# Performance work log

Measured on AMD Instinct MI355X. Metric: run time of the kernel, lower is better.

## Reference

```python
import jax, jax.numpy as jnp
import numpy as np

NH = 12      # bert-base heads
NL = 32      # num_latents
K = 64       # hard-coded topk in forward


def _ln(x, g, b):
    m = x.mean(-1, keepdims=True)
    v = ((x - m) ** 2).mean(-1, keepdims=True)
    return (x - m) / jnp.sqrt(v + 1e-12) * g + b


def _attn(xq, xkv, w, b, mask_add=None):
    # w: [4,H,H] (q,k,v,o), b: [4,H]
    B, Lq, H = xq.shape
    dh = H // NH
    q = (xq @ w[0] + b[0]).reshape(B, Lq, NH, dh)
    k = (xkv @ w[1] + b[1]).reshape(B, -1, NH, dh)
    v = (xkv @ w[2] + b[2]).reshape(B, -1, NH, dh)
    s = jnp.einsum('bqhd,bkhd->bhqk', q, k) / np.sqrt(dh).astype(xq.dtype)
    if mask_add is not None:
        s = s + mask_add
    p = jax.nn.softmax(s, axis=-1)          # [B,NH,Lq,Lk]
    o = jnp.einsum('bhqk,bkhd->bqhd', p, v).reshape(B, Lq, H)
    return o @ w[3] + b[3], p


def _cross_block(q, enc, w, b, g, lb, mask_add=None):
    # w:[L,8,H,H]; per layer: self-attn+LN then cross-attn+LN (FFN stripped)
    p_last = None
    for l in range(w.shape[0]):
        a, _ = _attn(q, q, w[l, :4], b[l, :4])
        q = _ln(q + a, g[l, 0], lb[l, 0])
        a, p_last = _attn(q, enc, w[l, 4:], b[l, 4:], mask_add)
        q = _ln(q + a, g[l, 1], lb[l, 1])
    return q, p_last


def _self_block(q, w, b, g, lb):
    probs = []
    for l in range(w.shape[0]):
        a, p = _attn(q, q, w[l], b[l])
        q = _ln(q + a, g[l, 0], lb[l, 0])
        probs.append(p)
    return q, jnp.concatenate(probs, axis=1)  # concat over head dim like torch.concat(attentions, dim=1)


def setup_inputs() -> dict:
    key = jax.random.key(0)
    ks = jax.random.split(key, 24)
    B, S, T, H, L = 32, 1024, 64, 768, 2
    std = 0.02
    inp = {
        'audio_embeds': jax.random.normal(ks[0], (B, S, H), jnp.float32),
        'text_embeds': jax.random.normal(ks[1], (B, T, H), jnp.float32),
        'attention_mask': jnp.ones((B, T), jnp.int32),
        'audio_qt': jax.random.normal(ks[2], (1, NL, H), jnp.float32) * std,
        'text_qt': jax.random.normal(ks[3], (1, NL, H), jnp.float32) * std,
    }
    for i, pre in enumerate(['tm', 'am', 'mg']):
        inp[pre + '_w'] = jax.random.normal(ks[4 + i], (L, 8, H, H), jnp.float32) * std
        inp[pre + '_b'] = jnp.zeros((L, 8, H), jnp.float32)
        inp[pre + '_g'] = jnp.ones((L, 2, H), jnp.float32)
        inp[pre + '_lb'] = jnp.zeros((L, 2, H), jnp.float32)
    inp['sel_w'] = jax.random.normal(ks[8], (L, 4, H, H), jnp.float32) * std
    inp['sel_b'] = jnp.zeros((L, 4, H), jnp.float32)
    inp['sel_g'] = jnp.ones((L, 1, H), jnp.float32)
    inp['sel_lb'] = jnp.zeros((L, 1, H), jnp.float32)
    return inp


def reference(audio_embeds, text_embeds, audio_qt, text_qt,
              tm_w, tm_b, tm_g, tm_lb, am_w, am_b, am_g, am_lb,
              sel_w, sel_b, sel_g, sel_lb, mg_w, mg_b, mg_g, mg_lb,
              attention_mask):
    B, S, H = audio_embeds.shape
    mask_add = (1.0 - attention_mask.astype(audio_embeds.dtype))[:, None, None, :] * -1e4

    # text token merger
    latent_text, _ = _cross_block(jnp.broadcast_to(text_qt, (B, NL, H)), text_embeds,
                                  tm_w, tm_b, tm_g, tm_lb, mask_add)
    # audio token merger (capture last-layer cross-attn probs)
    latent_audio, cross_p = _cross_block(jnp.broadcast_to(audio_qt, (B, NL, H)), audio_embeds,
                                         am_w, am_b, am_g, am_lb)
    latent_attention_score = cross_p.mean(axis=1)          # [B,NL,S]

    latent = jnp.concatenate([latent_audio, latent_text], axis=1)  # [B,2NL,H]
    fused, attn_all = _self_block(latent, sel_w, sel_b, sel_g, sel_lb)  # attn_all [B,L*NH,2NL,2NL]
    aas = attn_all[:, :, :NL, NL:].mean(axis=1)            # [B,NL,NL]

    imp = jnp.einsum('bqk,bks->bqs', aas, latent_attention_score).mean(axis=1)  # [B,S]
    _, idx = jax.lax.top_k(imp, K)
    sorted_idx = jnp.sort(idx, axis=1)                     # [B,K]

    sel_mask = jnp.zeros((B, S), bool).at[jnp.arange(B)[:, None], sorted_idx].set(True)
    q_tokens = jnp.take_along_axis(audio_embeds, sorted_idx[..., None], axis=1)  # [B,K,H]
    unsel_idx = jnp.argsort(sel_mask, axis=1, stable=True)[:, :S - K]            # order-preserving
    kv_rest = jnp.take_along_axis(audio_embeds, unsel_idx[..., None], axis=1)    # [B,S-K,H]
    kv = jnp.concatenate([kv_rest, fused], axis=1)                               # [B,S,H]

    out, _ = _cross_block(q_tokens, kv, mg_w, mg_b, mg_g, mg_lb)
    return out
```

## Files before the change

kernel.cpp:

```cpp
#include <hip/hip_runtime.h>
#include <hip/hip_bf16.h>
#include <math.h>

namespace {
constexpr int kB = 32, kS = 1024, kT = 64, kH = 768, kNH = 12, kDH = 64;
constexpr int kNL = 32, kTopK = 64, kL = 2;
constexpr size_t kMat = (size_t)kH * kH;
}

typedef _Float16 half8 __attribute__((ext_vector_type(8)));
typedef float floatx4 __attribute__((ext_vector_type(4)));

#define AS1U(p) ((const __attribute__((address_space(1))) unsigned int*)(p))
#define AS3U(p) ((__attribute__((address_space(3))) unsigned int*)(p))

__device__ __forceinline__ void split_write(float v, _Float16* H, _Float16* L, size_t i) {
    _Float16 h = (_Float16)v;
    H[i] = h;
    L[i] = (_Float16)(v - (float)h);
}

template<int NP>
__global__ __launch_bounds__(256) void gemm16(
    const _Float16* __restrict__ Aqh, const _Float16* __restrict__ Aql,
// ... 107 lines not shown
    const _Float16* __restrict__ Ah_, const _Float16* __restrict__ Al_,
    const _Float16* __restrict__ Bh_, const _Float16* __restrict__ Bl_,
    const float* __restrict__ bias, float* __restrict__ Y, int M)
{
    constexpr int NPL = (NP == 3) ? 4 : 2;
    __shared__ _Float16 lds[NPL * 4096];
    const int tid = threadIdx.x;
    const int lane = tid & 63, wave = tid >> 6;
    const size_t rm = (size_t)blockIdx.x * 128;
    const size_t cn = (size_t)blockIdx.y * 128;
    const int wr = (wave >> 1) * 64, wc = (wave & 1) * 64;

    const int lrow = lane >> 2;
    const int lchunk = (lane & 3) ^ ((lane >> 3) & 3);
    const int q = lane >> 4;
    const int fr = lane & 15;
    const int rslot = q ^ ((fr >> 1) & 3);

    const _Float16* gsrc;
    _Float16* lbase;
    int jbase;
    if constexpr (NP == 3) {
        gsrc = (wave == 0) ? Ah_ + rm * kH : (wave == 1) ? Al_ + rm * kH
             : (wave == 2) ? Bh_ + cn * kH : Bl_ + cn * kH;
        lbase = &lds[wave * 4096];
        jbase = 0;
    } else {
        gsrc = (wave < 2) ? Ah_ + rm * kH : Bh_ + cn * kH;
        lbase = &lds[(wave >> 1) * 4096];
        jbase = (wave & 1) * 4;
    }
    constexpr int CPW = (NP == 3) ? 8 : 4;

    floatx4 acc[4][4] = {};
    for (int k0 = 0; k0 < kH; k0 += 32) {
        #pragma unroll
        for (int c = 0; c < CPW; ++c) {
            int j = jbase + c;
            const _Float16* src = gsrc + (size_t)(j * 16 + lrow) * kH + k0 + lchunk * 8;
            _Float16* dst = lbase + j * 512 + lane * 8;
            __builtin_amdgcn_global_load_lds(AS1U(src), AS3U(dst), 16, 0, 0);
        }
        __syncthreads();
        half8 ah[4], bh[4], al[4], bl[4];
        #pragma unroll
        for (int m = 0; m < 4; ++m) {
            int r = wr + m * 16 + fr;
            ah[m] = *(const half8*)&lds[r * 32 + rslot * 8];
            if constexpr (NP == 3) al[m] = *(const half8*)&lds[4096 + r * 32 + rslot * 8];
        }
        constexpr int pb = (NP == 3) ? 2 : 1;
        #pragma unroll
        for (int n = 0; n < 4; ++n) {
            int r = wc + n * 16 + fr;
            bh[n] = *(const half8*)&lds[pb * 4096 + r * 32 + rslot * 8];
            if constexpr (NP == 3) bl[n] = *(const half8*)&lds[3 * 4096 + r * 32 + rslot * 8];
        }
        #pragma unroll
        for (int m = 0; m < 4; ++m)
            #pragma unroll
            for (int n = 0; n < 4; ++n) {
                acc[m][n] = __builtin_amdgcn_mfma_f32_16x16x32_f16(ah[m], bh[n], acc[m][n], 0, 0, 0);
                if constexpr (NP == 3) {
                    acc[m][n] = __builtin_amdgcn_mfma_f32_16x16x32_f16(ah[m], bl[n], acc[m][n], 0, 0, 0);
                    acc[m][n] = __builtin_amdgcn_mfma_f32_16x16x32_f16(al[m], bh[n], acc[m][n], 0, 0, 0);
                }
            }
        __syncthreads();
    }
    #pragma unroll
    for (int m = 0; m < 4; ++m) {
        int row0 = wr + m * 16 + (lane >> 4) * 4;
        #pragma unroll
        for (int n = 0; n < 4; ++n) {
            int col = (int)cn + wc + n * 16 + fr;
            float bv = bias[col];
            #pragma unroll
            for (int j = 0; j < 4; ++j)
                Y[(rm + row0 + j) * (size_t)kH + col] = acc[m][n][j] + bv;
        }
    }
}

template<int NP>
__global__ __launch_bounds__(256) void attn_big(
    const _Float16* __restrict__ Qh, const _Float16* __restrict__ Ql,
    const _Float16* __restrict__ Kh, const _Float16* __restrict__ Kl,
    float* __restrict__ P, int Lq, int Lk)
{
    constexpr int NPL = (NP == 3) ? 2 : 1;
    const int tid = threadIdx.x, lane = tid & 63, wave = tid >> 6;
    const int fr = lane & 15, part = lane >> 4;
    const int bh = blockIdx.x, b = bh / kNH, h = bh % kNH;
    const int q0 = blockIdx.y * 32;
    const int key0 = wave * 256;
    __shared__ float red[32][4];

    half8 qa[2][2][NPL];
    #pragma unroll
    for (int m = 0; m < 2; ++m)
        #pragma unroll
        for (int c = 0; c < 2; ++c) {
            size_t ro = (size_t)(b * Lq + q0 + m * 16 + fr) * kH + h * kDH + c * 32 + part * 8;
            qa[m][c][0] = *(const half8*)&Qh[ro];
            if constexpr (NP == 3) qa[m][c][1] = *(const half8*)&Ql[ro];
        }
    floatx4 acc[2][16] = {};
    #pragma unroll
    for (int n = 0; n < 16; ++n)
        #pragma unroll
        for (int c = 0; c < 2; ++c) {
            size_t ro = (size_t)(b * Lk + key0 + n * 16 + fr) * kH + h * kDH + c * 32 + part * 8;
            half8 kh8 = *(const half8*)&Kh[ro];
            half8 kl8;
            if constexpr (NP == 3) kl8 = *(const half8*)&Kl[ro];
            #pragma unroll
            for (int m = 0; m < 2; ++m) {
                acc[m][n] = __builtin_amdgcn_mfma_f32_16x16x32_f16(qa[m][c][0], kh8, acc[m][n], 0, 0, 0);
                if constexpr (NP == 3) {
                    acc[m][n] = __builtin_amdgcn_mfma_f32_16x16x32_f16(qa[m][c][0], kl8, acc[m][n], 0, 0, 0);
                    acc[m][n] = __builtin_amdgcn_mfma_f32_16x16x32_f16(qa[m][c][1], kh8, acc[m][n], 0, 0, 0);
                }
            }
        }
    #pragma unroll
    for (int m = 0; m < 2; ++m)
        #pragma unroll
        for (int n = 0; n < 16; ++n)
            #pragma unroll
            for (int j = 0; j < 4; ++j) acc[m][n][j] *= 0.125f;
    #pragma unroll
    for (int m = 0; m < 2; ++m)
        #pragma unroll
        for (int j = 0; j < 4; ++j) {
            float v = acc[m][0][j];
            #pragma unroll
            for (int n = 1; n < 16; ++n) v = fmaxf(v, acc[m][n][j]);
            #pragma unroll
            for (int o = 1; o < 16; o <<= 1) v = fmaxf(v, __shfl_xor(v, o));
            red[m * 16 + part * 4 + j][wave] = v;
        }
    __syncthreads();
    float gm[2][4];
    #pragma unroll
    for (int m = 0; m < 2; ++m)
        #pragma unroll
        for (int j = 0; j < 4; ++j) {
            int r = m * 16 + part * 4 + j;
            gm[m][j] = fmaxf(fmaxf(red[r][0], red[r][1]), fmaxf(red[r][2], red[r][3]));
        }
    __syncthreads();
    #pragma unroll
    for (int m = 0; m < 2; ++m)
        #pragma unroll
        for (int j = 0; j < 4; ++j) {
            float s = 0.f;
            #pragma unroll
            for (int n = 0; n < 16; ++n) {
                float e = expf(acc[m][n][j] - gm[m][j]);
                acc[m][n][j] = e;
                s += e;
            }
            #pragma unroll
            for (int o = 1; o < 16; o <<= 1) s += __shfl_xor(s, o);
            red[m * 16 + part * 4 + j][wave] = s;
        }
    __syncthreads();
    #pragma unroll
    for (int m = 0; m < 2; ++m)
        #pragma unroll
        for (int j = 0; j < 4; ++j) {
            int r = m * 16 + part * 4 + j;
            float inv = 1.0f / (red[r][0] + red[r][1] + red[r][2] + red[r][3]);
            size_t rowbase = ((size_t)bh * Lq + q0 + m * 16 + part * 4 + j) * Lk + key0;
            #pragma unroll
            for (int n = 0; n < 16; ++n)
                P[rowbase + n * 16 + fr] = acc[m][n][j] * inv;
        }
}

template<int LQ, int NP>
__global__ __launch_bounds__((LQ / 16) * 64) void pv_mfma(
    const float* __restrict__ P,
    const _Float16* __restrict__ Vh, const _Float16* __restrict__ Vl,
    _Float16* __restrict__ Oh, _Float16* __restrict__ Ol, int Lk)
{
    constexpr int NW = LQ / 16, NT = NW * 64;
    constexpr int NPL = (NP == 3) ? 2 : 1;
    __shared__ _Float16 vT[NPL][64][72];
    const int tid = threadIdx.x, lane = tid & 63, wave = tid >> 6;
    const int fr = lane & 15, part = lane >> 4;
    const int bh = blockIdx.x, b = bh / kNH, h = bh % kNH;
    const int qbase = wave * 16;

    floatx4 acc[4] = {};
    for (int kb = 0; kb < Lk; kb += 64) {
        for (int idx = tid; idx < 64 * 8; idx += NT) {
            int r = idx >> 3, c8 = idx & 7;
            half8 v = *(const half8*)&Vh[(size_t)(b * Lk + kb + r) * kH + h * kDH + c8 * 8];
            #pragma unroll
            for (int e = 0; e < 8; ++e) vT[0][c8 * 8 + e][r] = v[e];
            if constexpr (NP == 3) {
                half8 w = *(const half8*)&Vl[(size_t)(b * Lk + kb + r) * kH + h * kDH + c8 * 8];
                #pragma unroll
                for (int e = 0; e < 8; ++e) vT[1][c8 * 8 + e][r] = w[e];
            }
        }
        __syncthreads();
        half8 pa[2][NPL];
        #pragma unroll
        for (int c = 0; c < 2; ++c) {
            const float* src = &P[((size_t)bh * LQ + qbase + fr) * Lk + kb + c * 32 + part * 8];
            float4 x = *(const float4*)src, y = *(const float4*)(src + 4);
            float vv[8] = {x.x, x.y, x.z, x.w, y.x, y.y, y.z, y.w};
            #pragma unroll
            for (int e = 0; e < 8; ++e) {
                _Float16 hh = (_Float16)vv[e];
                pa[c][0][e] = hh;
                if constexpr (NP == 3) pa[c][1][e] = (_Float16)(vv[e] - (float)hh);
            }
        }
        #pragma unroll
        for (int n = 0; n < 4; ++n)
            #pragma unroll
            for (int c = 0; c < 2; ++c) {
                half8 bh8 = *(const half8*)&vT[0][n * 16 + fr][c * 32 + part * 8];
                acc[n] = __builtin_amdgcn_mfma_f32_16x16x32_f16(pa[c][0], bh8, acc[n], 0, 0, 0);
                if constexpr (NP == 3) {
                    half8 bl8 = *(const half8*)&vT[1][n * 16 + fr][c * 32 + part * 8];
                    acc[n] = __builtin_amdgcn_mfma_f32_16x16x32_f16(pa[c][0], bl8, acc[n], 0, 0, 0);
                    acc[n] = __builtin_amdgcn_mfma_f32_16x16x32_f16(pa[c][1], bh8, acc[n], 0, 0, 0);
                }
            }
        __syncthreads();
    }
    #pragma unroll
    for (int n = 0; n < 4; ++n)
        #pragma unroll
        for (int j = 0; j < 4; ++j) {
            size_t oi = (size_t)(b * LQ + qbase + part * 4 + j) * kH + h * kDH + n * 16 + fr;
            float v = acc[n][j];
            _Float16 hh = (_Float16)v;
            Oh[oi] = hh;
            if constexpr (NP == 3) Ol[oi] = (_Float16)(v - (float)hh);
        }
}

template<int LQ, int LK, int NP, bool MASKED, bool CAPTURE>
__global__ __launch_bounds__((LQ / 16) * 64) void attn_small(
    const _Float16* Qh, const _Float16* Ql,
    const _Float16* __restrict__ Kh, const _Float16* __restrict__ Kl,
    const _Float16* __restrict__ Vh, const _Float16* __restrict__ Vl,
    _Float16* Oh, _Float16* Ol,
    float* __restrict__ Pcap, const int* __restrict__ amask)
{
    constexpr int NW = LQ / 16, NT = NW * 64, NN = LK / 16, NC = LK / 32;
    constexpr int NPL = (NP == 3) ? 2 : 1;
    constexpr int PIT = LK + 8;
    __shared__ _Float16 vT[NPL][64][PIT];
    __shared__ _Float16 Pld[NW][NPL][16][PIT];
    const int tid = threadIdx.x, lane = tid & 63, wave = tid >> 6;
    const int fr = lane & 15, part = lane >> 4;
    const int bh = blockIdx.x, b = bh / kNH, h = bh % kNH;

    for (int idx = tid; idx < LK * 8; idx += NT) {
        int r = idx >> 3, c8 = idx & 7;
        half8 v = *(const half8*)&Vh[(size_t)(b * LK + r) * kH + h * kDH + c8 * 8];
        #pragma unroll
        for (int e = 0; e < 8; ++e) vT[0][c8 * 8 + e][r] = v[e];
        if constexpr (NP == 3) {
            half8 w = *(const half8*)&Vl[(size_t)(b * LK + r) * kH + h * kDH + c8 * 8];
            #pragma unroll
            for (int e = 0; e < 8; ++e) vT[1][c8 * 8 + e][r] = w[e];
        }
    }
    half8 qa[2][NPL];
    #pragma unroll
    for (int c = 0; c < 2; ++c) {
        size_t ro = (size_t)(b * LQ + wave * 16 + fr) * kH + h * kDH + c * 32 + part * 8;
        qa[c][0] = *(const half8*)&Qh[ro];
        if constexpr (NP == 3) qa[c][1] = *(const half8*)&Ql[ro];
    }
    floatx4 acc[NN] = {};
    #pragma unroll
    for (int n = 0; n < NN; ++n)
        #pragma unroll
        for (int c = 0; c < 2; ++c) {
            size_t ro = (size_t)(b * LK + n * 16 + fr) * kH + h * kDH + c * 32 + part * 8;
            half8 kh8 = *(const half8*)&Kh[ro];
            acc[n] = __builtin_amdgcn_mfma_f32_16x16x32_f16(qa[c][0], kh8, acc[n], 0, 0, 0);
            if constexpr (NP == 3) {
                half8 kl8 = *(const half8*)&Kl[ro];
                acc[n] = __builtin_amdgcn_mfma_f32_16x16x32_f16(qa[c][0], kl8, acc[n], 0, 0, 0);
                acc[n] = __builtin_amdgcn_mfma_f32_16x16x32_f16(qa[c][1], kh8, acc[n], 0, 0, 0);
            }
        }
    #pragma unroll
    for (int n = 0; n < NN; ++n) {
        float madd = 0.f;
        if constexpr (MASKED)
            madd = (1.0f - (float)amask[b * kT + n * 16 + fr]) * -1e4f;
        #pragma unroll
        for (int j = 0; j < 4; ++j) acc[n][j] = acc[n][j] * 0.125f + madd;
    }
    #pragma unroll
    for (int j = 0; j < 4; ++j) {
        float m = acc[0][j];
        #pragma unroll
        for (int n = 1; n < NN; ++n) m = fmaxf(m, acc[n][j]);
        #pragma unroll
        for (int o = 1; o < 16; o <<= 1) m = fmaxf(m, __shfl_xor(m, o));
        float s = 0.f;
        #pragma unroll
        for (int n = 0; n < NN; ++n) { float e = expf(acc[n][j] - m); acc[n][j] = e; s += e; }
        #pragma unroll
        for (int o = 1; o < 16; o <<= 1) s += __shfl_xor(s, o);
        float inv = 1.0f / s;
        #pragma unroll
        for (int n = 0; n < NN; ++n) acc[n][j] *= inv;
    }
    #pragma unroll
    for (int n = 0; n < NN; ++n)
        #pragma unroll
        for (int j = 0; j < 4; ++j) {
// ... 205 lines not shown
    for (int c = threadIdx.x; c < kH; c += 256) {
        float v = qt[(size_t)n * kH + c];
        q[(size_t)bn * kH + c] = v;
        split_write(v, Qh, Ql, (size_t)bn * kH + c);
    }
}

__global__ __launch_bounds__(256) void concat_lat(const float* __restrict__ qa,
    const float* __restrict__ qt, float* __restrict__ lat,
    _Float16* __restrict__ Lh, _Float16* __restrict__ Ll)
{
    const int br = blockIdx.x;
    const int b = br >> 6, r = br & 63;
    const float* src = (r < kNL) ? qa + (size_t)(b * kNL + r) * kH
                                 : qt + (size_t)(b * kNL + (r - kNL)) * kH;
    for (int c = threadIdx.x; c < kH; c += 256) {
        float v = src[c];
        lat[(size_t)br * kH + c] = v;
        split_write(v, Lh, Ll, (size_t)br * kH + c);
    }
}

__global__ __launch_bounds__(256) void gather_q(const float* __restrict__ audio,
    const int* __restrict__ selidx, float* __restrict__ qm,
    _Float16* __restrict__ Qh, _Float16* __restrict__ Ql)
{
    const int bj = blockIdx.x;
    const int b = bj >> 6;
    const int srow = selidx[bj];
    const float* src = audio + ((size_t)b * kS + srow) * kH;
    for (int c = threadIdx.x; c < kH; c += 256) {
        float v = src[c];
        qm[(size_t)bj * kH + c] = v;
        split_write(v, Qh, Ql, (size_t)bj * kH + c);
    }
}

__global__ __launch_bounds__(256) void build_kv(const float* __restrict__ audio,
    const float* __restrict__ fused, const int* __restrict__ unselidx,
    _Float16* __restrict__ Kh, _Float16* __restrict__ Kl)
{
    const int br = blockIdx.x;
    const int b = br >> 10, r = br & 1023;
    const float* src;
    if (r < kS - kTopK) src = audio + ((size_t)b * kS + unselidx[b * (kS - kTopK) + r]) * kH;
    else                src = fused + (size_t)(b * kTopK + (r - (kS - kTopK))) * kH;
    for (int c = threadIdx.x; c < kH; c += 256)
        split_write(src[c], Kh, Kl, (size_t)br * kH + c);
}

extern "C" void kernel_launch(void* const* d_in, const int* in_sizes, int n_in,
                              void* d_out, int out_size, void* d_ws, size_t ws_size,
                              hipStream_t stream)
{
    const float* audio    = (const float*)d_in[0];
    const float* text     = (const float*)d_in[1];
    const int*   amask    = (const int*)  d_in[2];
    const float* audio_qt = (const float*)d_in[3];
    const float* text_qt  = (const float*)d_in[4];
    const float* tm_w  = (const float*)d_in[5];
    const float* tm_b  = (const float*)d_in[6];
    const float* tm_g  = (const float*)d_in[7];
    const float* tm_lb = (const float*)d_in[8];
    const float* am_w  = (const float*)d_in[9];
    const float* am_b  = (const float*)d_in[10];
    const float* am_g  = (const float*)d_in[11];
    const float* am_lb = (const float*)d_in[12];
    const float* mg_w  = (const float*)d_in[13];
    const float* mg_b  = (const float*)d_in[14];
    const float* mg_g  = (const float*)d_in[15];
    const float* mg_lb = (const float*)d_in[16];
    const float* sel_w  = (const float*)d_in[17];
    const float* sel_b  = (const float*)d_in[18];
    const float* sel_g  = (const float*)d_in[19];
    const float* sel_lb = (const float*)d_in[20];
    (void)in_sizes; (void)n_in; (void)out_size;

    char* base = (char*)d_ws;
    size_t off = 0;
    auto alloc = [&](size_t bytes) {
        off = (off + 255) & ~(size_t)255;
        void* p = base + off; off += bytes; return p;
    };
    float* Pbuf   = (float*)alloc((size_t)kB * kNH * 64 * kS * 4);
    float* attA   = (float*)alloc((size_t)2048 * kH * 4);
    float* q_text = (float*)alloc((size_t)1024 * kH * 4);
    float* q_audio= (float*)alloc((size_t)1024 * kH * 4);
    float* latent = (float*)alloc((size_t)2048 * kH * 4);
    float* qmerge = (float*)alloc((size_t)2048 * kH * 4);
    float* latsc  = (float*)alloc((size_t)kB * kNL * kS * 4);
    float* aas    = (float*)alloc((size_t)kB * kNL * kNL * 4);
    float* impb   = (float*)alloc((size_t)kB * kS * 4);
    int* selidx   = (int*)alloc((size_t)kB * kTopK * 4);
    int* unselidx = (int*)alloc((size_t)kB * (kS - kTopK) * 4);
    _Float16* Wh  = (_Float16*)alloc(16 * kMat * 2);
    _Float16* Wl  = (_Float16*)alloc(16 * kMat * 2);
    _Float16* BGh = (_Float16*)alloc((size_t)kB * kS * kH * 2);
    _Float16* BGl = (_Float16*)alloc((size_t)kB * kS * kH * 2);
    _Float16* PTh = (_Float16*)alloc((size_t)kB * kT * kH * 2);
    _Float16* PTl = (_Float16*)alloc((size_t)kB * kT * kH * 2);
    _Float16* PLqh= (_Float16*)alloc((size_t)2048 * kH * 2);
    _Float16* PLql= (_Float16*)alloc((size_t)2048 * kH * 2);
    _Float16* PLoh= (_Float16*)alloc((size_t)2048 * kH * 2);
    _Float16* PLol= (_Float16*)alloc((size_t)2048 * kH * 2);
    _Float16* KVh = (_Float16*)alloc((size_t)kB * kS * kH * 2);
    _Float16* KVl = (_Float16*)alloc((size_t)kB * kS * kH * 2);
    if (off > ws_size) return;

    _Float16* Qh = PLoh;
    _Float16* Ql = PLol;

    auto attn = [&](const float* qf, int Lq,
                    const _Float16* qah, const _Float16* qal,
                    const _Float16* eah, const _Float16* eal, int Lk,
                    int wmat, const float* bias, const float* g, const float* lb,
                    const int* mask, int capture, bool np3,
                    float* q_out, _Float16* oh, _Float16* ol)
    {
        const int Mq = kB * Lq, Mk = kB * Lk;
        const _Float16* WhB = Wh + (size_t)wmat * kMat;
        const _Float16* WlB = Wl + (size_t)wmat * kMat;
        const int gx = (Mq > Mk ? Mq : Mk) / 128;
        if (Lk >= 256) {
            dim3 g1(gx, 6, 2);
            if (np3) gemm16<3><<<g1, 256, 0, stream>>>(qah, qal, eah, eal, WhB, WlB, bias,
                         Qh, Ql, KVh, KVl, nullptr, nullptr, Mq, Mk);
            else     gemm16<1><<<g1, 256, 0, stream>>>(qah, qal, eah, eal, WhB, WlB, bias,
                         Qh, Ql, KVh, KVl, nullptr, nullptr, Mq, Mk);
            dim3 g2(kB * kNH, Lq / 32);
            if (np3) attn_big<3><<<g2, 256, 0, stream>>>(Qh, Ql, KVh, KVl, Pbuf, Lq, Lk);
            else     attn_big<1><<<g2, 256, 0, stream>>>(Qh, Ql, KVh, KVl, Pbuf, Lq, Lk);
            if (capture == 1) mean_heads<<<kB * kNL, 256, 0, stream>>>(Pbuf, latsc);
            dim3 g3(Mk / 128, 6, 1);
            if (np3) gemm16<3><<<g3, 256, 0, stream>>>(eah, eal, eah, eal,
                         WhB + 2 * kMat, WlB + 2 * kMat, bias + 2 * kH,
                         KVh, KVl, nullptr, nullptr, nullptr, nullptr, Mk, Mk);
            else     gemm16<1><<<g3, 256, 0, stream>>>(eah, eal, eah, eal,
                         WhB + 2 * kMat, WlB + 2 * kMat, bias + 2 * kH,
                         KVh, KVl, nullptr, nullptr, nullptr, nullptr, Mk, Mk);
            if (Lq == 32) {
                if (np3) pv_mfma<32, 3><<<kB * kNH, 128, 0, stream>>>(Pbuf, KVh, KVl, PLoh, PLol, Lk);
                else     pv_mfma<32, 1><<<kB * kNH, 128, 0, stream>>>(Pbuf, KVh, KVl, PLoh, PLol, Lk);
            } else {
                if (np3) pv_mfma<64, 3><<<kB * kNH, 256, 0, stream>>>(Pbuf, KVh, KVl, PLoh, PLol, Lk);
                else     pv_mfma<64, 1><<<kB * kNH, 256, 0, stream>>>(Pbuf, KVh, KVl, PLoh, PLol, Lk);
            }
        } else {
            _Float16* V2h = KVh + (size_t)Mk * kH;
            _Float16* V2l = KVl + (size_t)Mk * kH;
            dim3 g1(gx, 6, 3);
            if (np3) gemm16<3><<<g1, 256, 0, stream>>>(qah, qal, eah, eal, WhB, WlB, bias,
                         Qh, Ql, KVh, KVl, V2h, V2l, Mq, Mk);
            else     gemm16<1><<<g1, 256, 0, stream>>>(qah, qal, eah, eal, WhB, WlB, bias,
                         Qh, Ql, KVh, KVl, V2h, V2l, Mq, Mk);
            if (Lq == 32 && Lk == 32)
                attn_small<32, 32, 3, false, false><<<kB * kNH, 128, 0, stream>>>(
                    Qh, Ql, KVh, KVl, V2h, V2l, PLoh, PLol, nullptr, nullptr);
            else if (Lq == 32 && Lk == 64)
                attn_small<32, 64, 3, true, false><<<kB * kNH, 128, 0, stream>>>(
                    Qh, Ql, KVh, KVl, V2h, V2l, PLoh, PLol, nullptr, mask);
            else if (np3)
                attn_small<64, 64, 3, false, true><<<kB * kNH, 256, 0, stream>>>(
                    Qh, Ql, KVh, KVl, V2h, V2l, PLoh, PLol, Pbuf, nullptr);
            else
                attn_small<64, 64, 1, false, false><<<kB * kNH, 256, 0, stream>>>(
                    Qh, Ql, KVh, KVl, V2h, V2l, PLoh, PLol, nullptr, nullptr);
            if (capture == 2)      aas_acc<<<kB, 256, 0, stream>>>(Pbuf, aas, 1);
            else if (capture == 3) aas_acc<<<kB, 256, 0, stream>>>(Pbuf, aas, 0);
        }
        dim3 g4(Mq / 128, 6);
        if (np3) gemm_o32<3><<<g4, 256, 0, stream>>>(PLoh, PLol, WhB + 3 * kMat, WlB + 3 * kMat,
                     bias + 3 * kH, attA, Mq);
        else     gemm_o32<1><<<g4, 256, 0, stream>>>(PLoh, PLol, WhB + 3 * kMat, WlB + 3 * kMat,
                     bias + 3 * kH, attA, Mq);
        ln_residual<<<Mq, 256, 0, stream>>>(qf, attA, g, lb, q_out, oh, ol);
    };

    split2<<<(kB * kT * kH) / 1024, 256, 0, stream>>>(text, PTh, PTl, kB * kT * kH);
    split2<<<(kB * kS * kH) / 1024, 256, 0, stream>>>(audio, BGh, BGl, kB * kS * kH);

    wconv<<<dim3(24, 24, 16), 256, 0, stream>>>(tm_w, Wh, Wl);
    bcast_q<<<kB * kNL, 256, 0, stream>>>(text_qt, q_text, PLqh, PLql);
    for (int l = 0; l < kL; ++l) {
        attn(q_text, kNL, PLqh, PLql, PLqh, PLql, kNL, l * 8 + 0,
             tm_b + (size_t)l * 8 * kH, tm_g + (size_t)l * 2 * kH, tm_lb + (size_t)l * 2 * kH,
             nullptr, 0, true, q_text, PLqh, PLql);
        attn(q_text, kNL, PLqh, PLql, PTh, PTl, kT, l * 8 + 4,
             tm_b + ((size_t)l * 8 + 4) * kH, tm_g + ((size_t)l * 2 + 1) * kH, tm_lb + ((size_t)l * 2 + 1) * kH,
             amask, 0, true, q_text, PLqh, PLql);
    }
    wconv<<<dim3(24, 24, 16), 256, 0, stream>>>(am_w, Wh, Wl);
    bcast_q<<<kB * kNL, 256, 0, stream>>>(audio_qt, q_audio, PLqh, PLql);
    for (int l = 0; l < kL; ++l) {
        attn(q_audio, kNL, PLqh, PLql, PLqh, PLql, kNL, l * 8 + 0,
             am_b + (size_t)l * 8 * kH, am_g + (size_t)l * 2 * kH, am_lb + (size_t)l * 2 * kH,
             nullptr, 0, true, q_audio, PLqh, PLql);
        attn(q_audio, kNL, PLqh, PLql, BGh, BGl, kS, l * 8 + 4,
             am_b + ((size_t)l * 8 + 4) * kH, am_g + ((size_t)l * 2 + 1) * kH, am_lb + ((size_t)l * 2 + 1) * kH,
             nullptr, (l == kL - 1) ? 1 : 0, true, q_audio, PLqh, PLql);
    }
    concat_lat<<<kB * 64, 256, 0, stream>>>(q_audio, q_text, latent, PLqh, PLql);
    wconv<<<dim3(24, 24, 8), 256, 0, stream>>>(sel_w, Wh, Wl);
    for (int l = 0; l < kL; ++l) {
        attn(latent, 64, PLqh, PLql, PLqh, PLql, 64, l * 4,
             sel_b + (size_t)l * 4 * kH, sel_g + (size_t)l * kH, sel_lb + (size_t)l * kH,
             nullptr, (l == 0) ? 2 : 3, true, latent, PLqh, PLql);
    }
    imp_kernel<<<kB, 256, 0, stream>>>(aas, latsc, impb);
    topk_kernel<<<kB, 256, 0, stream>>>(impb, selidx, unselidx);
    gather_q<<<kB * kTopK, 256, 0, stream>>>(audio, selidx, qmerge, PLqh, PLql);
    build_kv<<<kB * kS, 256, 0, stream>>>(audio, latent, unselidx, BGh, BGl);
    wconv<<<dim3(24, 24, 16), 256, 0, stream>>>(mg_w, Wh, Wl);
    for (int l = 0; l < kL; ++l) {
        attn(qmerge, 64, PLqh, PLql, PLqh, PLql, 64, l * 8 + 0,
             mg_b + (size_t)l * 8 * kH, mg_g + (size_t)l * 2 * kH, mg_lb + (size_t)l * 2 * kH,
             nullptr, 0, false, qmerge, PLqh, PLql);
        float* qo = (l == kL - 1) ? (float*)d_out : qmerge;
        _Float16* oh = (l == kL - 1) ? nullptr : PLqh;
        _Float16* ol = (l == kL - 1) ? nullptr : PLql;
        attn(qmerge, 64, PLqh, PLql, BGh, BGl, kS, l * 8 + 4,
             mg_b + ((size_t)l * 8 + 4) * kH, mg_g + ((size_t)l * 2 + 1) * kH, mg_lb + ((size_t)l * 2 + 1) * kH,
             nullptr, 0, false, qo, oh, ol);
    }
}
```

Measured before the change: 2.338 ms.

## Reassociate cross-attention to skip K/V projections of the long sequence

For the two cross-attention stages over the 1024-token sequence, the K and V projections of the encoder sequence are replaced by reassociated products. The per-head query is folded through Wk (R = Q_h·Wk_hᵀ) and scored directly against the raw encoder embeddings. P is multiplied by the raw embeddings first and then by Wv. This removes the large Mk×768×768 K and V GEMMs in exchange for per-head 64×768 intermediates and extra small GEMMs. K-bias is dropped, which is valid because it shifts every score in a row equally, and V-bias is added after the projection, which is valid because softmax rows sum to one. The merge stage also stores P in fp16 to halve its traffic, which may change accuracy.

```diff
diff --git a/kernel.cpp b/kernel.cpp
--- a/kernel.cpp
+++ b/kernel.cpp
@@ -213,47 +213,96 @@
     }
 }
 
-template<int NP>
-__global__ __launch_bounds__(256) void attn_big(
+template<int LQ, int NP>
+__global__ __launch_bounds__(256) void rgemm(
     const _Float16* __restrict__ Qh, const _Float16* __restrict__ Ql,
-    const _Float16* __restrict__ Kh, const _Float16* __restrict__ Kl,
-    float* __restrict__ P, int Lq, int Lk)
-{
-    constexpr int NPL = (NP == 3) ? 2 : 1;
+    const _Float16* __restrict__ Wnh, const _Float16* __restrict__ Wnl,
+    _Float16* __restrict__ Rh, _Float16* __restrict__ Rl)
+{
+    constexpr int MM = LQ / 16;
     const int tid = threadIdx.x, lane = tid & 63, wave = tid >> 6;
     const int fr = lane & 15, part = lane >> 4;
     const int bh = blockIdx.x, b = bh / kNH, h = bh % kNH;
+    const int ncol = blockIdx.y * 64 + wave * 16;
+
+    half8 qa[MM][2][2];
+    #pragma unroll
+    for (int m = 0; m < MM; ++m)
+        #pragma unroll
+        for (int c = 0; c < 2; ++c) {
+            size_t ro = (size_t)(b * LQ + m * 16 + fr) * kH + h * kDH + c * 32 + part * 8;
+            qa[m][c][0] = *(const half8*)&Qh[ro];
+            if constexpr (NP == 3) qa[m][c][1] = *(const half8*)&Ql[ro];
+        }
+    floatx4 acc[MM] = {};
+    #pragma unroll
+    for (int c = 0; c < 2; ++c) {
+        size_t ro = (size_t)(ncol + fr) * kH + h * kDH + c * 32 + part * 8;
+        half8 wb = *(const half8*)&Wnh[ro];
+        half8 wl;
+        if constexpr (NP == 3) wl = *(const half8*)&Wnl[ro];
+        #pragma unroll
+        for (int m = 0; m < MM; ++m) {
+            acc[m] = __builtin_amdgcn_mfma_f32_16x16x32_f16(qa[m][c][0], wb, acc[m], 0, 0, 0);
+            if constexpr (NP == 3) {
+                acc[m] = __builtin_amdgcn_mfma_f32_16x16x32_f16(qa[m][c][0], wl, acc[m], 0, 0, 0);
+                acc[m] = __builtin_amdgcn_mfma_f32_16x16x32_f16(qa[m][c][1], wb, acc[m], 0, 0, 0);
+            }
+        }
+    }
+    #pragma unroll
+    for (int m = 0; m < MM; ++m)
+        #pragma unroll
+        for (int j = 0; j < 4; ++j) {
+            size_t oi = (size_t)(bh * LQ + m * 16 + part * 4 + j) * kH + ncol + fr;
+            float v = acc[m][j];
+            _Float16 hh = (_Float16)v;
+            Rh[oi] = hh;
+            if constexpr (NP == 3) Rl[oi] = (_Float16)(v - (float)hh);
+        }
+}
+
+template<int NP, bool PF16>
+__global__ __launch_bounds__(256) void scores_rx(
+    const _Float16* __restrict__ Rh, const _Float16* __restrict__ Rl,
+    const _Float16* __restrict__ Xh, const _Float16* __restrict__ Xl,
+    float* __restrict__ P32, _Float16* __restrict__ P16, int Lq)
+{
+    const int tid = threadIdx.x, lane = tid & 63, wave = tid >> 6;
+    const int fr = lane & 15, part = lane >> 4;
+    const int i = blockIdx.x;
+    const int b = (i & 7) * 4 + ((i >> 3) & 3);
+    const int h = i >> 5;
+    const int bh = b * kNH + h;
     const int q0 = blockIdx.y * 32;
     const int key0 = wave * 256;
     __shared__ float red[32][4];
 
-    half8 qa[2][2][NPL];
-    #pragma unroll
-    for (int m = 0; m < 2; ++m)
-        #pragma unroll
-        for (int c = 0; c < 2; ++c) {
-            size_t ro = (size_t)(b * Lq + q0 + m * 16 + fr) * kH + h * kDH + c * 32 + part * 8;
-            qa[m][c][0] = *(const half8*)&Qh[ro];
-            if constexpr (NP == 3) qa[m][c][1] = *(const half8*)&Ql[ro];
-        }
     floatx4 acc[2][16] = {};
-    #pragma unroll
-    for (int n = 0; n < 16; ++n)
-        #pragma unroll
-        for (int c = 0; c < 2; ++c) {
-            size_t ro = (size_t)(b * Lk + key0 + n * 16 + fr) * kH + h * kDH + c * 32 + part * 8;
-            half8 kh8 = *(const half8*)&Kh[ro];
-            half8 kl8;
-            if constexpr (NP == 3) kl8 = *(const half8*)&Kl[ro];
+    for (int c = 0; c < 24; ++c) {
+        half8 ah[2][2];
+        #pragma unroll
+        for (int m = 0; m < 2; ++m) {
+            size_t ro = (size_t)(bh * Lq + q0 + m * 16 + fr) * kH + c * 32 + part * 8;
+            ah[m][0] = *(const half8*)&Rh[ro];
+            if constexpr (NP == 3) ah[m][1] = *(const half8*)&Rl[ro];
+        }
+        #pragma unroll
+        for (int n = 0; n < 16; ++n) {
+            size_t ro = (size_t)(b * kS + key0 + n * 16 + fr) * kH + c * 32 + part * 8;
+            half8 bh8 = *(const half8*)&Xh[ro];
+            half8 bl8;
+            if constexpr (NP == 3) bl8 = *(const half8*)&Xl[ro];
             #pragma unroll
             for (int m = 0; m < 2; ++m) {
-                acc[m][n] = __builtin_amdgcn_mfma_f32_16x16x32_f16(qa[m][c][0], kh8, acc[m][n], 0, 0, 0);
+                acc[m][n] = __builtin_amdgcn_mfma_f32_16x16x32_f16(ah[m][0], bh8, acc[m][n], 0, 0, 0);
                 if constexpr (NP == 3) {
-                    acc[m][n] = __builtin_amdgcn_mfma_f32_16x16x32_f16(qa[m][c][0], kl8, acc[m][n], 0, 0, 0);
-                    acc[m][n] = __builtin_amdgcn_mfma_f32_16x16x32_f16(qa[m][c][1], kh8, acc[m][n], 0, 0, 0);
+                    acc[m][n] = __builtin_amdgcn_mfma_f32_16x16x32_f16(ah[m][0], bl8, acc[m][n], 0, 0, 0);
+                    acc[m][n] = __builtin_amdgcn_mfma_f32_16x16x32_f16(ah[m][1], bh8, acc[m][n], 0, 0, 0);
                 }
             }
         }
+    }
     #pragma unroll
     for (int m = 0; m < 2; ++m)
         #pragma unroll
@@ -303,74 +352,138 @@
         for (int j = 0; j < 4; ++j) {
             int r = m * 16 + part * 4 + j;
             float inv = 1.0f / (red[r][0] + red[r][1] + red[r][2] + red[r][3]);
-            size_t rowbase = ((size_t)bh * Lq + q0 + m * 16 + part * 4 + j) * Lk + key0;
-            #pragma unroll
-            for (int n = 0; n < 16; ++n)
-                P[rowbase + n * 16 + fr] = acc[m][n][j] * inv;
-        }
+            size_t rowbase = ((size_t)bh * Lq + q0 + m * 16 + part * 4 + j) * kS + key0;
+            #pragma unroll
+            for (int n = 0; n < 16; ++n) {
+                float p = acc[m][n][j] * inv;
+                if constexpr (PF16) P16[rowbase + n * 16 + fr] = (_Float16)p;
+                else                P32[rowbase + n * 16 + fr] = p;
+            }
+        }
+}
+
+template<int LQ, int NP, bool PF16>
+__global__ __launch_bounds__(256) void zgemm(
+    const float* __restrict__ P32, const _Float16* __restrict__ P16,
+    const _Float16* __restrict__ Xh, const _Float16* __restrict__ Xl,
+    _Float16* __restrict__ Zh, _Float16* __restrict__ Zl)
+{
+    constexpr int MM = LQ / 16;
+    constexpr int NPL = (NP == 3) ? 2 : 1;
+    __shared__ _Float16 xT[NPL][128][72];
+    const int tid = threadIdx.x, lane = tid & 63, wave = tid >> 6;
+    const int fr = lane & 15, part = lane >> 4;
+    const int i = blockIdx.x;
+    const int b = (i & 7) * 4 + ((i >> 3) & 3);
+    const int r2 = i >> 5;
+    const int h = r2 % kNH, nt = r2 / kNH;
+    const int bh = b * kNH + h;
+
+    floatx4 acc[MM][2] = {};
+    for (int kb = 0; kb < 16; ++kb) {
+        for (int idx = tid; idx < 64 * 16; idx += 256) {
+            int key = idx >> 4, cg = idx & 15;
+            size_t ro = (size_t)(b * kS + kb * 64 + key) * kH + nt * 128 + cg * 8;
+            half8 v = *(const half8*)&Xh[ro];
+            #pragma unroll
+            for (int e = 0; e < 8; ++e) xT[0][cg * 8 + e][key] = v[e];
+            if constexpr (NP == 3) {
+                half8 w = *(const half8*)&Xl[ro];
+                #pragma unroll
+                for (int e = 0; e < 8; ++e) xT[1][cg * 8 + e][key] = w[e];
+            }
+        }
+        __syncthreads();
+        #pragma unroll
+        for (int c2 = 0; c2 < 2; ++c2) {
+            half8 pa[MM][2];
+            #pragma unroll
+            for (int m = 0; m < MM; ++m) {
+                if constexpr (PF16) {
+                    size_t ro = (size_t)(bh * LQ + m * 16 + fr) * kS + kb * 64 + c2 * 32 + part * 8;
+                    pa[m][0] = *(const half8*)&P16[ro];
+                } else {
+                    const float* src = &P32[(size_t)(bh * LQ + m * 16 + fr) * kS + kb * 64 + c2 * 32 + part * 8];
+                    float4 x = *(const float4*)src, y = *(const float4*)(src + 4);
+                    float vv[8] = {x.x, x.y, x.z, x.w, y.x, y.y, y.z, y.w};
+                    #pragma unroll
+                    for (int e = 0; e < 8; ++e) {
+                        _Float16 hh = (_Float16)vv[e];
+                        pa[m][0][e] = hh;
+                        if constexpr (NP == 3) pa[m][1][e] = (_Float16)(vv[e] - (float)hh);
+                    }
+                }
+            }
+            #pragma unroll
+            for (int nf = 0; nf < 2; ++nf) {
+                int col = wave * 32 + nf * 16 + fr;
+                half8 bh8 = *(const half8*)&xT[0][col][c2 * 32 + part * 8];
+                half8 bl8;
+                if constexpr (NP == 3) bl8 = *(const half8*)&xT[1][col][c2 * 32 + part * 8];
+                #pragma unroll
+                for (int m = 0; m < MM; ++m) {
+                    acc[m][nf] = __builtin_amdgcn_mfma_f32_16x16x32_f16(pa[m][0], bh8, acc[m][nf], 0, 0, 0);
+                    if constexpr (NP == 3) {
+                        acc[m][nf] = __builtin_amdgcn_mfma_f32_16x16x32_f16(pa[m][0], bl8, acc[m][nf], 0, 0, 0);
+                        acc[m][nf] = __builtin_amdgcn_mfma_f32_16x16x32_f16(pa[m][1], bh8, acc[m][nf], 0, 0, 0);
+                    }
+                }
+            }
+        }
+        __syncthreads();
+    }
+    #pragma unroll
+    for (int m = 0; m < MM; ++m)
+        #pragma unroll
+        for (int nf = 0; nf < 2; ++nf)
+            #pragma unroll
+            for (int j = 0; j < 4; ++j) {
+                size_t oi = (size_t)(bh * LQ + m * 16 + part * 4 + j) * kH + nt * 128 + wave * 32 + nf * 16 + fr;
+                float v = acc[m][nf][j];
+                _Float16 hh = (_Float16)v;
+                Zh[oi] = hh;
+                if constexpr (NP == 3) Zl[oi] = (_Float16)(v - (float)hh);
+            }
 }
 
 template<int LQ, int NP>
-__global__ __launch_bounds__((LQ / 16) * 64) void pv_mfma(
-    const float* __restrict__ P,
-    const _Float16* __restrict__ Vh, const _Float16* __restrict__ Vl,
-    _Float16* __restrict__ Oh, _Float16* __restrict__ Ol, int Lk)
-{
-    constexpr int NW = LQ / 16, NT = NW * 64;
-    constexpr int NPL = (NP == 3) ? 2 : 1;
-    __shared__ _Float16 vT[NPL][64][72];
+__global__ __launch_bounds__(256) void ogemm(
+    const _Float16* __restrict__ Zh, const _Float16* __restrict__ Zl,
+    const _Float16* __restrict__ WTh, const _Float16* __restrict__ WTl,
+    const float* __restrict__ bv,
+    _Float16* __restrict__ Oh, _Float16* __restrict__ Ol)
+{
+    constexpr int MM = LQ / 16;
     const int tid = threadIdx.x, lane = tid & 63, wave = tid >> 6;
     const int fr = lane & 15, part = lane >> 4;
     const int bh = blockIdx.x, b = bh / kNH, h = bh % kNH;
-    const int qbase = wave * 16;
-
-    floatx4 acc[4] = {};
-    for (int kb = 0; kb < Lk; kb += 64) {
-        for (int idx = tid; idx < 64 * 8; idx += NT) {
-            int r = idx >> 3, c8 = idx & 7;
-            half8 v = *(const half8*)&Vh[(size_t)(b * Lk + kb + r) * kH + h * kDH + c8 * 8];
-            #pragma unroll
-            for (int e = 0; e < 8; ++e) vT[0][c8 * 8 + e][r] = v[e];
+    const int colbase = h * kDH + wave * 16;
+
+    floatx4 acc[MM] = {};
+    for (int c = 0; c < 24; ++c) {
+        size_t wo = (size_t)(colbase + fr) * kH + c * 32 + part * 8;
+        half8 wb = *(const half8*)&WTh[wo];
+        half8 wl;
+        if constexpr (NP == 3) wl = *(const half8*)&WTl[wo];
+        #pragma unroll
+        for (int m = 0; m < MM; ++m) {
+            size_t ro = (size_t)(bh * LQ + m * 16 + fr) * kH + c * 32 + part * 8;
+            half8 ah = *(const half8*)&Zh[ro];
+            acc[m] = __builtin_amdgcn_mfma_f32_16x16x32_f16(ah, wb, acc[m], 0, 0, 0);
             if constexpr (NP == 3) {
-                half8 w = *(const half8*)&Vl[(size_t)(b * Lk + kb + r) * kH + h * kDH + c8 * 8];
-                #pragma unroll
-                for (int e = 0; e < 8; ++e) vT[1][c8 * 8 + e][r] = w[e];
-            }
-        }
-        __syncthreads();
-        half8 pa[2][NPL];
-        #pragma unroll
-        for (int c = 0; c < 2; ++c) {
-            const float* src = &P[((size_t)bh * LQ + qbase + fr) * Lk + kb + c * 32 + part * 8];
-            float4 x = *(const float4*)src, y = *(const float4*)(src + 4);
-            float vv[8] = {x.x, x.y, x.z, x.w, y.x, y.y, y.z, y.w};
-            #pragma unroll
-            for (int e = 0; e < 8; ++e) {
-                _Float16 hh = (_Float16)vv[e];
-                pa[c][0][e] = hh;
-                if constexpr (NP == 3) pa[c][1][e] = (_Float16)(vv[e] - (float)hh);
-            }
-        }
-        #pragma unroll
-        for (int n = 0; n < 4; ++n)
-            #pragma unroll
-            for (int c = 0; c < 2; ++c) {
-                half8 bh8 = *(const half8*)&vT[0][n * 16 + fr][c * 32 + part * 8];
-                acc[n] = __builtin_amdgcn_mfma_f32_16x16x32_f16(pa[c][0], bh8, acc[n], 0, 0, 0);
-                if constexpr (NP == 3) {
-                    half8 bl8 = *(const half8*)&vT[1][n * 16 + fr][c * 32 + part * 8];
-                    acc[n] = __builtin_amdgcn_mfma_f32_16x16x32_f16(pa[c][0], bl8, acc[n], 0, 0, 0);
-                    acc[n] = __builtin_amdgcn_mfma_f32_16x16x32_f16(pa[c][1], bh8, acc[n], 0, 0, 0);
-                }
-            }
-        __syncthreads();
-    }
-    #pragma unroll
-    for (int n = 0; n < 4; ++n)
+                half8 al = *(const half8*)&Zl[ro];
+                acc[m] = __builtin_amdgcn_mfma_f32_16x16x32_f16(ah, wl, acc[m], 0, 0, 0);
+                acc[m] = __builtin_amdgcn_mfma_f32_16x16x32_f16(al, wb, acc[m], 0, 0, 0);
+            }
+        }
+    }
+    float bias = bv[colbase + fr];
+    #pragma unroll
+    for (int m = 0; m < MM; ++m)
         #pragma unroll
         for (int j = 0; j < 4; ++j) {
-            size_t oi = (size_t)(b * LQ + qbase + part * 4 + j) * kH + h * kDH + n * 16 + fr;
-            float v = acc[n][j];
+            size_t oi = (size_t)(b * LQ + m * 16 + part * 4 + j) * kH + colbase + fr;
+            float v = acc[m][j] + bias;
             _Float16 hh = (_Float16)v;
             Oh[oi] = hh;
             if constexpr (NP == 3) Ol[oi] = (_Float16)(v - (float)hh);
@@ -742,7 +855,7 @@
         off = (off + 255) & ~(size_t)255;
         void* p = base + off; off += bytes; return p;
     };
-    float* Pbuf   = (float*)alloc((size_t)kB * kNH * 64 * kS * 4);
+    float* Pbuf   = (float*)alloc((size_t)kB * kNH * 32 * kS * 4);
     float* attA   = (float*)alloc((size_t)2048 * kH * 4);
     float* q_text = (float*)alloc((size_t)1024 * kH * 4);
     float* q_audio= (float*)alloc((size_t)1024 * kH * 4);
@@ -755,6 +868,8 @@
     int* unselidx = (int*)alloc((size_t)kB * (kS - kTopK) * 4);
     _Float16* Wh  = (_Float16*)alloc(16 * kMat * 2);
     _Float16* Wl  = (_Float16*)alloc(16 * kMat * 2);
+    _Float16* WkNh= (_Float16*)alloc(2 * kMat * 2);
+    _Float16* WkNl= (_Float16*)alloc(2 * kMat * 2);
     _Float16* BGh = (_Float16*)alloc((size_t)kB * kS * kH * 2);
     _Float16* BGl = (_Float16*)alloc((size_t)kB * kS * kH * 2);
     _Float16* PTh = (_Float16*)alloc((size_t)kB * kT * kH * 2);
@@ -763,8 +878,10 @@
     _Float16* PLql= (_Float16*)alloc((size_t)2048 * kH * 2);
     _Float16* PLoh= (_Float16*)alloc((size_t)2048 * kH * 2);
     _Float16* PLol= (_Float16*)alloc((size_t)2048 * kH * 2);
-    _Float16* KVh = (_Float16*)alloc((size_t)kB * kS * kH * 2);
-    _Float16* KVl = (_Float16*)alloc((size_t)kB * kS * kH * 2);
+    _Float16* KVh = (_Float16*)alloc((size_t)2 * 2048 * kH * 2);
+    _Float16* KVl = (_Float16*)alloc((size_t)2 * 2048 * kH * 2);
+    _Float16* ZRh = (_Float16*)alloc((size_t)kB * kNH * 64 * kH * 2);
+    _Float16* ZRl = (_Float16*)alloc((size_t)kB * kNH * 64 * kH * 2);
     if (off > ws_size) return;
 
     _Float16* Qh = PLoh;
@@ -781,53 +898,70 @@
         const _Float16* WhB = Wh + (size_t)wmat * kMat;
         const _Float16* WlB = Wl + (size_t)wmat * kMat;
         const int gx = (Mq > Mk ? Mq : Mk) / 128;
-        if (Lk >= 256) {
-            dim3 g1(gx, 6, 2);
-            if (np3) gemm16<3><<<g1, 256, 0, stream>>>(qah, qal, eah, eal, WhB, WlB, bias,
-                         Qh, Ql, KVh, KVl, nullptr, nullptr, Mq, Mk);
-            else     gemm16<1><<<g1, 256, 0, stream>>>(qah, qal, eah, eal, WhB, WlB, bias,
-                         Qh, Ql, KVh, KVl, nullptr, nullptr, Mq, Mk);
-            dim3 g2(kB * kNH, Lq / 32);
-            if (np3) attn_big<3><<<g2, 256, 0, stream>>>(Qh, Ql, KVh, KVl, Pbuf, Lq, Lk);
-            else     attn_big<1><<<g2, 256, 0, stream>>>(Qh, Ql, KVh, KVl, Pbuf, Lq, Lk);
-            if (capture == 1) mean_heads<<<kB * kNL, 256, 0, stream>>>(Pbuf, latsc);
-            dim3 g3(Mk / 128, 6, 1);
-            if (np3) gemm16<3><<<g3, 256, 0, stream>>>(eah, eal, eah, eal,
-                         WhB + 2 * kMat, WlB + 2 * kMat, bias + 2 * kH,
-                         KVh, KVl, nullptr, nullptr, nullptr, nullptr, Mk, Mk);
-            else     gemm16<1><<<g3, 256, 0, stream>>>(eah, eal, eah, eal,
-                         WhB + 2 * kMat, WlB + 2 * kMat, bias + 2 * kH,
-                         KVh, KVl, nullptr, nullptr, nullptr, nullptr, Mk, Mk);
-            if (Lq == 32) {
-                if (np3) pv_mfma<32, 3><<<kB * kNH, 128, 0, stream>>>(Pbuf, KVh, KVl, PLoh, PLol, Lk);
-                else     pv_mfma<32, 1><<<kB * kNH, 128, 0, stream>>>(Pbuf, KVh, KVl, PLoh, PLol, Lk);
-            } else {
-                if (np3) pv_mfma<64, 3><<<kB * kNH, 256, 0, stream>>>(Pbuf, KVh, KVl, PLoh, PLol, Lk);
-                else     pv_mfma<64, 1><<<kB * kNH, 256, 0, stream>>>(Pbuf, KVh, KVl, PLoh, PLol, Lk);
-            }
-        } else {
-            _Float16* V2h = KVh + (size_t)Mk * kH;
-            _Float16* V2l = KVl + (size_t)Mk * kH;
-            dim3 g1(gx, 6, 3);
-            if (np3) gemm16<3><<<g1, 256, 0, stream>>>(qah, qal, eah, eal, WhB, WlB, bias,
-                         Qh, Ql, KVh, KVl, V2h, V2l, Mq, Mk);
-            else     gemm16<1><<<g1, 256, 0, stream>>>(qah, qal, eah, eal, WhB, WlB, bias,
-                         Qh, Ql, KVh, KVl, V2h, V2l, Mq, Mk);
-            if (Lq == 32 && Lk == 32)
-                attn_small<32, 32, 3, false, false><<<kB * kNH, 128, 0, stream>>>(
-                    Qh, Ql, KVh, KVl, V2h, V2l, PLoh, PLol, nullptr, nullptr);
-            else if (Lq == 32 && Lk == 64)
-                attn_small<32, 64, 3, true, false><<<kB * kNH, 128, 0, stream>>>(
-                    Qh, Ql, KVh, KVl, V2h, V2l, PLoh, PLol, nullptr, mask);
-            else if (np3)
-                attn_small<64, 64, 3, false, true><<<kB * kNH, 256, 0, stream>>>(
-                    Qh, Ql, KVh, KVl, V2h, V2l, PLoh, PLol, Pbuf, nullptr);
-            else
-                attn_small<64, 64, 1, false, false><<<kB * kNH, 256, 0, stream>>>(
-                    Qh, Ql, KVh, KVl, V2h, V2l, PLoh, PLol, nullptr, nullptr);
-            if (capture == 2)      aas_acc<<<kB, 256, 0, stream>>>(Pbuf, aas, 1);
-            else if (capture == 3) aas_acc<<<kB, 256, 0, stream>>>(Pbuf, aas, 0);
-        }
+        _Float16* V2h = KVh + (size_t)Mk * kH;
+        _Float16* V2l = KVl + (size_t)Mk * kH;
+        dim3 g1(gx, 6, 3);
+        if (np3) gemm16<3><<<g1, 256, 0, stream>>>(qah, qal, eah, eal, WhB, WlB, bias,
+                     Qh, Ql, KVh, KVl, V2h, V2l, Mq, Mk);
+        else     gemm16<1><<<g1, 256, 0, stream>>>(qah, qal, eah, eal, WhB, WlB, bias,
+                     Qh, Ql, KVh, KVl, V2h, V2l, Mq, Mk);
+        if (Lq == 32 && Lk == 32)
+            attn_small<32, 32, 3, false, false><<<kB * kNH, 128, 0, stream>>>(
+                Qh, Ql, KVh, KVl, V2h, V2l, PLoh, PLol, nullptr, nullptr);
+        else if (Lq == 32 && Lk == 64)
+            attn_small<32, 64, 3, true, false><<<kB * kNH, 128, 0, stream>>>(
+                Qh, Ql, KVh, KVl, V2h, V2l, PLoh, PLol, nullptr, mask);
+        else if (np3)
+            attn_small<64, 64, 3, false, true><<<kB * kNH, 256, 0, stream>>>(
+                Qh, Ql, KVh, KVl, V2h, V2l, PLoh, PLol, Pbuf, nullptr);
+        else
+            attn_small<64, 64, 1, false, false><<<kB * kNH, 256, 0, stream>>>(
+                Qh, Ql, KVh, KVl, V2h, V2l, PLoh, PLol, nullptr, nullptr);
+        if (capture == 2)      aas_acc<<<kB, 256, 0, stream>>>(Pbuf, aas, 1);
+        else if (capture == 3) aas_acc<<<kB, 256, 0, stream>>>(Pbuf, aas, 0);
+        dim3 g4(Mq / 128, 6);
+        if (np3) gemm_o32<3><<<g4, 256, 0, stream>>>(PLoh, PLol, WhB + 3 * kMat, WlB + 3 * kMat,
+                     bias + 3 * kH, attA, Mq);
+        else     gemm_o32<1><<<g4, 256, 0, stream>>>(PLoh, PLol, WhB + 3 * kMat, WlB + 3 * kMat,
+                     bias + 3 * kH, attA, Mq);
+        ln_residual<<<Mq, 256, 0, stream>>>(qf, attA, g, lb, q_out, oh, ol);
+    };
+
+    auto big_step = [&](const float* qf, int Lq,
+                        const _Float16* qah, const _Float16* qal,
+                        int wmat, int kl, const float* bias,
+                        const float* g, const float* lb,
+                        int capture, bool np3,
+                        float* q_out, _Float16* oh, _Float16* ol)
+    {
+        const int Mq = kB * Lq;
+        const _Float16* WhB = Wh + (size_t)wmat * kMat;
+        const _Float16* WlB = Wl + (size_t)wmat * kMat;
+        dim3 gq(Mq / 128, 6, 1);
+        if (np3) gemm16<3><<<gq, 256, 0, stream>>>(qah, qal, qah, qal, WhB, WlB, bias,
+                     Qh, Ql, nullptr, nullptr, nullptr, nullptr, Mq, Mq);
+        else     gemm16<1><<<gq, 256, 0, stream>>>(qah, qal, qah, qal, WhB, WlB, bias,
+                     Qh, Ql, nullptr, nullptr, nullptr, nullptr, Mq, Mq);
+        dim3 gr(kB * kNH, 12);
+        if (np3) rgemm<32, 3><<<gr, 256, 0, stream>>>(Qh, Ql, WkNh + (size_t)kl * kMat,
+                     WkNl + (size_t)kl * kMat, ZRh, ZRl);
+        else     rgemm<64, 1><<<gr, 256, 0, stream>>>(Qh, Ql, WkNh + (size_t)kl * kMat,
+                     WkNl + (size_t)kl * kMat, ZRh, ZRl);
+        dim3 gs(kB * kNH, Lq / 32);
+        if (np3) scores_rx<3, false><<<gs, 256, 0, stream>>>(ZRh, ZRl, BGh, BGl,
+                     Pbuf, nullptr, Lq);
+        else     scores_rx<1, true><<<gs, 256, 0, stream>>>(ZRh, ZRl, BGh, BGl,
+                     nullptr, (_Float16*)Pbuf, Lq);
+        if (capture == 1) mean_heads<<<kB * kNL, 256, 0, stream>>>(Pbuf, latsc);
+        dim3 gz(2304);
+        if (np3) zgemm<32, 3, false><<<gz, 256, 0, stream>>>(Pbuf, nullptr, BGh, BGl, ZRh, ZRl);
+        else     zgemm<64, 1, true><<<gz, 256, 0, stream>>>(nullptr, (const _Float16*)Pbuf,
+                     BGh, BGl, ZRh, ZRl);
+        dim3 go(kB * kNH);
+        if (np3) ogemm<32, 3><<<go, 256, 0, stream>>>(ZRh, ZRl, WhB + 2 * kMat, WlB + 2 * kMat,
+                     bias + 2 * kH, PLoh, PLol);
+        else     ogemm<64, 1><<<go, 256, 0, stream>>>(ZRh, ZRl, WhB + 2 * kMat, WlB + 2 * kMat,
+                     bias + 2 * kH, PLoh, PLol);
         dim3 g4(Mq / 128, 6);
         if (np3) gemm_o32<3><<<g4, 256, 0, stream>>>(PLoh, PLol, WhB + 3 * kMat, WlB + 3 * kMat,
                      bias + 3 * kH, attA, Mq);
@@ -850,14 +984,17 @@
              amask, 0, true, q_text, PLqh, PLql);
     }
     wconv<<<dim3(24, 24, 16), 256, 0, stream>>>(am_w, Wh, Wl);
+    for (int l = 0; l < kL; ++l)
+        split2<<<(int)(kMat / 1024), 256, 0, stream>>>(am_w + ((size_t)l * 8 + 5) * kMat,
+            WkNh + (size_t)l * kMat, WkNl + (size_t)l * kMat, (int)kMat);
     bcast_q<<<kB * kNL, 256, 0, stream>>>(audio_qt, q_audio, PLqh, PLql);
     for (int l = 0; l < kL; ++l) {
         attn(q_audio, kNL, PLqh, PLql, PLqh, PLql, kNL, l * 8 + 0,
              am_b + (size_t)l * 8 * kH, am_g + (size_t)l * 2 * kH, am_lb + (size_t)l * 2 * kH,
              nullptr, 0, true, q_audio, PLqh, PLql);
-        attn(q_audio, kNL, PLqh, PLql, BGh, BGl, kS, l * 8 + 4,
+        big_step(q_audio, kNL, PLqh, PLql, l * 8 + 4, l,
              am_b + ((size_t)l * 8 + 4) * kH, am_g + ((size_t)l * 2 + 1) * kH, am_lb + ((size_t)l * 2 + 1) * kH,
-             nullptr, (l == kL - 1) ? 1 : 0, true, q_audio, PLqh, PLql);
+             (l == kL - 1) ? 1 : 0, true, q_audio, PLqh, PLql);
     }
     concat_lat<<<kB * 64, 256, 0, stream>>>(q_audio, q_text, latent, PLqh, PLql);
     wconv<<<dim3(24, 24, 8), 256, 0, stream>>>(sel_w, Wh, Wl);
@@ -871,6 +1008,9 @@
     gather_q<<<kB * kTopK, 256, 0, stream>>>(audio, selidx, qmerge, PLqh, PLql);
     build_kv<<<kB * kS, 256, 0, stream>>>(audio, latent, unselidx, BGh, BGl);
     wconv<<<dim3(24, 24, 16), 256, 0, stream>>>(mg_w, Wh, Wl);
+    for (int l = 0; l < kL; ++l)
+        split2<<<(int)(kMat / 1024), 256, 0, stream>>>(mg_w + ((size_t)l * 8 + 5) * kMat,
+            WkNh + (size_t)l * kMat, WkNl + (size_t)l * kMat, (int)kMat);
     for (int l = 0; l < kL; ++l) {
         attn(qmerge, 64, PLqh, PLql, PLqh, PLql, 64, l * 8 + 0,
              mg_b + (size_t)l * 8 * kH, mg_g + (size_t)l * 2 * kH, mg_lb + (size_t)l * 2 * kH,
@@ -878,8 +1018,8 @@
         float* qo = (l == kL - 1) ? (float*)d_out : qmerge;
         _Float16* oh = (l == kL - 1) ? nullptr : PLqh;
         _Float16* ol = (l == kL - 1) ? nullptr : PLql;
-        attn(qmerge, 64, PLqh, PLql, BGh, BGl, kS, l * 8 + 4,
+        big_step(qmerge, 64, PLqh, PLql, l * 8 + 4, l,
              mg_b + ((size_t)l * 8 + 4) * kH, mg_g + ((size_t)l * 2 + 1) * kH, mg_lb + ((size_t)l * 2 + 1) * kH,
-             nullptr, 0, false, qo, oh, ol);
-    }
-}
+             0, false, qo, oh, ol);
+    }
+}
```

Measured after the change: 4.223 ms. 80.6% more time.
